# Kernel tuning notes

Hardware: AMD Instinct MI355X
Metric: run time of the kernel (lower is better)

Reference implementation:

```python
import jax, jax.numpy as jnp
import numpy as np

TOKEN_DIM = 4
EPS = 1e-6


def setup_inputs() -> dict:
    key = jax.random.key(0)
    k_x, k_w = jax.random.split(key)
    B, S, E = 8, 8192, 512
    EMB = 512
    x = jax.random.normal(k_x, (B, S, E), dtype=jnp.float32)
    ln_gamma = jnp.ones((E,), dtype=jnp.float32)
    ln_beta = jnp.zeros((E,), dtype=jnp.float32)
    # glorot-ish scale for the compression kernel [token_dim*E, EMB]
    W = jax.random.normal(k_w, (TOKEN_DIM * E, EMB), dtype=jnp.float32) * 0.02
    b = jnp.zeros((EMB,), dtype=jnp.float32)
    return {"x": x, "ln_gamma": ln_gamma, "ln_beta": ln_beta, "W": W, "b": b}


def reference(x, ln_gamma, ln_beta, W, b):
    B, S, E = x.shape
    # LayerNormalization over the feature axis (center + scale)
    mean = jnp.mean(x, axis=-1, keepdims=True)
    var = jnp.mean(jnp.square(x - mean), axis=-1, keepdims=True)
    h = (x - mean) * jax.lax.rsqrt(var + EPS) * ln_gamma + ln_beta
    # Divide: split sequence axis by token_dim and merge factor into feature axis
    # [B, S, E] -> [B, S//T, T*E]
    h = h.reshape(B, S // TOKEN_DIM, TOKEN_DIM * E)
    # Dense compression + exact gelu (keras 'gelu' uses erf form)
    out = jnp.einsum('bsf,fd->bsd', h, W) + b
    return jax.nn.gelu(out, approximate=False)
```

## Files before the change

kernel.cpp:

```cpp
#include <hip/hip_runtime.h>
#include <hip/hip_bf16.h>
#include <cstdint>

#define XROWS   65536
#define E       512
#define MROWS   16384
#define KDIM    2048
#define NDIM    512

typedef __attribute__((ext_vector_type(4))) float f32x4;
typedef __attribute__((ext_vector_type(8))) unsigned short u16x8;
typedef __attribute__((ext_vector_type(8))) __bf16 bf16x8;

__device__ __forceinline__ unsigned short f2bf(float f) {
  unsigned u = __builtin_bit_cast(unsigned, f);
  u += 0x7FFFu + ((u >> 16) & 1u);
  return (unsigned short)(u >> 16);
}

typedef const __attribute__((address_space(1))) unsigned char ga_u8;
typedef __attribute__((address_space(3))) unsigned char ls_u8;
__device__ __forceinline__ void gload16(const void* g, void* l) {
  __builtin_amdgcn_global_load_lds((ga_u8*)g, (ls_u8*)l, 16, 0, 0);
}

__global__ __launch_bounds__(256) void wt_kernel(const float* __restrict__ W,
                                                 unsigned short* __restrict__ WT) {
  __shared__ float tile[64][68];
  const int t  = threadIdx.x;
  const int bk = blockIdx.x >> 3;
  const int bn = blockIdx.x & 7;
  const int c4 = (t & 15) * 4;
#pragma unroll
  for (int i = 0; i < 4; ++i) {
    const int r = (t >> 4) + i * 16;
    const f32x4 v = *(const f32x4*)&W[(size_t)(bk * 64 + r) * NDIM + bn * 64 + c4];
    tile[r][c4 + 0] = v.x; tile[r][c4 + 1] = v.y;
    tile[r][c4 + 2] = v.z; tile[r][c4 + 3] = v.w;
  }
  __syncthreads();
#pragma unroll
  for (int j = 0; j < 2; ++j) {
    const int n  = j * 32 + (t >> 3);
    const int kb = (t & 7) * 8;
    u16x8 o;
#pragma unroll
    for (int q = 0; q < 8; ++q) o[q] = f2bf(tile[kb + q][n]);
    *(u16x8*)&WT[(size_t)(bn * 64 + n) * KDIM + bk * 64 + kb] = o;
  }
}

__global__ __launch_bounds__(256, 4) void ln_kernel(const float* __restrict__ x,
                                                    const float* __restrict__ gamma,
                                                    const float* __restrict__ beta,
                                                    unsigned short* __restrict__ h) {
  const int w = threadIdx.x >> 6, l = threadIdx.x & 63;
  const size_t row = (size_t)blockIdx.x * 4 + w;
  const float* xr = x + row * E + l * 8;
  const f32x4 v0 = *(const f32x4*)xr;
  const f32x4 v1 = *(const f32x4*)(xr + 4);
  float xv[8] = {v0.x, v0.y, v0.z, v0.w, v1.x, v1.y, v1.z, v1.w};
  float s = 0.f, q = 0.f;
#pragma unroll
  for (int j = 0; j < 8; ++j) { s += xv[j]; q += xv[j] * xv[j]; }
#pragma unroll
  for (int off = 32; off > 0; off >>= 1) {
    s += __shfl_xor(s, off);
    q += __shfl_xor(q, off);
  }
  const float mean = s * (1.0f / E);
  const float var  = q * (1.0f / E) - mean * mean;
  const float rstd = rsqrtf(var + 1e-6f);
  const f32x4 g0 = *(const f32x4*)(gamma + l * 8);
  const f32x4 g1 = *(const f32x4*)(gamma + l * 8 + 4);
  const f32x4 b0 = *(const f32x4*)(beta + l * 8);
  const f32x4 b1 = *(const f32x4*)(beta + l * 8 + 4);
  const float gv[8] = {g0.x, g0.y, g0.z, g0.w, g1.x, g1.y, g1.z, g1.w};
  const float bv[8] = {b0.x, b0.y, b0.z, b0.w, b1.x, b1.y, b1.z, b1.w};
  u16x8 o;
#pragma unroll
  for (int j = 0; j < 8; ++j) o[j] = f2bf((xv[j] - mean) * rstd * gv[j] + bv[j]);
  *(u16x8*)(h + row * E + l * 8) = o;
}

#define NT (KDIM / 64)

__global__ __launch_bounds__(256, 2) void gemm_kernel(const unsigned short* __restrict__ A,
                                                      const unsigned short* __restrict__ Bt,
                                                      const float* __restrict__ bias,
                                                      float* __restrict__ out) {
  __shared__ char smem[2 * 32768];
  const int tid = threadIdx.x;
  const int l = tid & 63, w = tid >> 6;
  const int l7 = l & 7, l15 = l & 15, lhi = l >> 4;
  const int wr = w >> 1, wc = w & 1;

  const int bn = blockIdx.x & 3;
  const int bm = blockIdx.x >> 2;
  const size_t arow0 = (size_t)bm * 128;
  const int    brow0 = bn * 128;

  const int srow = w * 8 + (l >> 3);
  const int swz  = (l7 * 16) ^ ((l >> 3) << 4);
  const char* gAb = (const char*)A  + ((size_t)(arow0 + srow) * KDIM) * 2 + swz;
  const char* gBb = (const char*)Bt + ((size_t)(brow0 + srow) * KDIM) * 2 + swz;

  auto stage = [&](int buf, int t) {
    char* base = smem + buf * 32768;
    const char* pa = gAb + (size_t)t * 128;
    const char* pb = gBb + (size_t)t * 128;
#pragma unroll
    for (int i = 0; i < 4; ++i) {
      gload16(pa + (size_t)i * 32 * KDIM * 2, base + (i * 32 + w * 8) * 128);
      gload16(pb + (size_t)i * 32 * KDIM * 2, base + 16384 + (i * 32 + w * 8) * 128);
    }
  };

  f32x4 acc[4][4];
#pragma unroll
  for (int m = 0; m < 4; ++m)
#pragma unroll
    for (int n = 0; n < 4; ++n) acc[m][n] = (f32x4){0.f, 0.f, 0.f, 0.f};

  const int cs0 = (lhi * 16) ^ (l7 * 16);

  stage(0, 0);
  __syncthreads();

  for (int t = 0; t < NT; ++t) {
    if (t + 1 < NT) stage((t + 1) & 1, t + 1);
    const char* Ab = smem + (t & 1) * 32768;
    const char* Bb = Ab + 16384;
#pragma unroll
    for (int kk = 0; kk < 2; ++kk) {
      const int co = cs0 ^ (kk * 64);
      bf16x8 av[4], bv[4];
#pragma unroll
      for (int m = 0; m < 4; ++m)
        av[m] = *(const bf16x8*)(Ab + (wr * 64 + m * 16 + l15) * 128 + co);
#pragma unroll
      for (int n = 0; n < 4; ++n)
        bv[n] = *(const bf16x8*)(Bb + (wc * 64 + n * 16 + l15) * 128 + co);
#pragma unroll
      for (int m = 0; m < 4; ++m)
#pragma unroll
        for (int n = 0; n < 4; ++n)
          acc[m][n] = __builtin_amdgcn_mfma_f32_16x16x32_bf16(av[m], bv[n], acc[m][n], 0, 0, 0);
    }
    __syncthreads();
  }

#pragma unroll
  for (int n = 0; n < 4; ++n) {
    const int col = brow0 + wc * 64 + n * 16 + l15;
    const float bb = bias[col];
#pragma unroll
    for (int m = 0; m < 4; ++m) {
      const size_t rbase = arow0 + wr * 64 + m * 16 + lhi * 4;
#pragma unroll
      for (int r = 0; r < 4; ++r) {
        const float v = acc[m][n][r] + bb;
        const float ge = 0.5f * v * (1.0f + erff(v * 0.70710678118654752f));
        out[(rbase + r) * NDIM + col] = ge;
      }
    }
  }
}

extern "C" void kernel_launch(void* const* d_in, const int* in_sizes, int n_in,
                              void* d_out, int out_size, void* d_ws, size_t ws_size,
                              hipStream_t stream) {
  const float* x     = (const float*)d_in[0];
  const float* gamma = (const float*)d_in[1];
  const float* beta  = (const float*)d_in[2];
  const float* W     = (const float*)d_in[3];
  const float* bias  = (const float*)d_in[4];
  float* out = (float*)d_out;

  unsigned short* WT = (unsigned short*)d_ws;
  const size_t wtBytes = (size_t)NDIM * KDIM * 2;
  unsigned short* h = (unsigned short*)((char*)d_ws + wtBytes);

  int NC = 1;
  while (NC < 64 && wtBytes + ((size_t)MROWS / NC) * KDIM * 2 > ws_size) NC <<= 1;
  const int Mc = MROWS / NC;

  wt_kernel<<<256, 256, 0, stream>>>(W, WT);
  for (int c = 0; c < NC; ++c) {
    const float* xc = x + (size_t)c * Mc * KDIM;
    ln_kernel<<<Mc, 256, 0, stream>>>(xc, gamma, beta, h);
    gemm_kernel<<<(Mc / 128) * 4, 256, 0, stream>>>(h, WT, bias,
                                                    out + (size_t)c * Mc * NDIM);
  }
}
```

Measured before the change: 87.92 us.

## Fuse LayerNorm apply into GEMM A-load, fold gamma/beta into weights and bias

The LayerNorm is split: a stats kernel writes only per-row scale and shift, and the GEMM loads fp32 x directly, normalizes and converts to bf16 into LDS while B streams in asynchronously. Gamma is folded into the transposed bf16 weights and beta@W plus b into a precomputed bias, so the bf16 h intermediate no longer has to be written and re-read. The GEMM tile changes to 64x256 with a register double-buffered A prefetch. The exact erf GELU is replaced by a sigmoid-style exp2 approximation, which is cheaper but may lose accuracy.

Measured after the change: 115.8 us. 31.7% more time.

```diff
diff --git a/kernel.cpp b/kernel.cpp
--- a/kernel.cpp
+++ b/kernel.cpp
@@ -7,8 +7,10 @@
 #define MROWS   16384
 #define KDIM    2048
 #define NDIM    512
+#define NT      32
 
 typedef __attribute__((ext_vector_type(4))) float f32x4;
+typedef __attribute__((ext_vector_type(2))) float f32x2;
 typedef __attribute__((ext_vector_type(8))) unsigned short u16x8;
 typedef __attribute__((ext_vector_type(8))) __bf16 bf16x8;
 
@@ -24,7 +26,15 @@
   __builtin_amdgcn_global_load_lds((ga_u8*)g, (ls_u8*)l, 16, 0, 0);
 }
 
+__device__ __forceinline__ float gelu_f(float v) {
+  float p = v * (2.3022083f + 0.1029432f * (v * v));
+  p = fminf(p, 80.0f);
+  const float Ee = exp2f(p);
+  return v * Ee * __builtin_amdgcn_rcpf(Ee + 1.0f);
+}
+
 __global__ __launch_bounds__(256) void wt_kernel(const float* __restrict__ W,
+                                                 const float* __restrict__ gamma,
                                                  unsigned short* __restrict__ WT) {
   __shared__ float tile[64][68];
   const int t  = threadIdx.x;
@@ -43,78 +53,89 @@
   for (int j = 0; j < 2; ++j) {
     const int n  = j * 32 + (t >> 3);
     const int kb = (t & 7) * 8;
+    const int kg0 = (bk & 7) * 64 + kb;
+    const f32x4 g0 = *(const f32x4*)(gamma + kg0);
+    const f32x4 g1 = *(const f32x4*)(gamma + kg0 + 4);
+    const float gg[8] = {g0.x, g0.y, g0.z, g0.w, g1.x, g1.y, g1.z, g1.w};
     u16x8 o;
 #pragma unroll
-    for (int q = 0; q < 8; ++q) o[q] = f2bf(tile[kb + q][n]);
+    for (int q = 0; q < 8; ++q) o[q] = f2bf(gg[q] * tile[kb + q][n]);
     *(u16x8*)&WT[(size_t)(bn * 64 + n) * KDIM + bk * 64 + kb] = o;
   }
 }
 
-__global__ __launch_bounds__(256, 4) void ln_kernel(const float* __restrict__ x,
-                                                    const float* __restrict__ gamma,
-                                                    const float* __restrict__ beta,
-                                                    unsigned short* __restrict__ h) {
+__global__ __launch_bounds__(256) void kbias1(const float* __restrict__ W,
+                                              const float* __restrict__ beta,
+                                              float* __restrict__ partial) {
+  const int bk = blockIdx.x, tid = threadIdx.x;
+  float a0 = 0.f, a1 = 0.f;
+  for (int k = 0; k < 64; ++k) {
+    const int kg = bk * 64 + k;
+    const float be = beta[kg & (E - 1)];
+    a0 += be * W[(size_t)kg * NDIM + tid];
+    a1 += be * W[(size_t)kg * NDIM + 256 + tid];
+  }
+  partial[bk * NDIM + tid] = a0;
+  partial[bk * NDIM + 256 + tid] = a1;
+}
+
+__global__ __launch_bounds__(256) void kbias2(const float* __restrict__ b,
+                                              const float* __restrict__ partial,
+                                              float* __restrict__ biasf) {
+  const int c = blockIdx.x * 256 + threadIdx.x;
+  float s = b[c];
+  for (int j = 0; j < 32; ++j) s += partial[j * NDIM + c];
+  biasf[c] = s;
+}
+
+__global__ __launch_bounds__(256, 4) void stats_kernel(const float* __restrict__ x,
+                                                       f32x2* __restrict__ stats) {
   const int w = threadIdx.x >> 6, l = threadIdx.x & 63;
   const size_t row = (size_t)blockIdx.x * 4 + w;
   const float* xr = x + row * E + l * 8;
   const f32x4 v0 = *(const f32x4*)xr;
   const f32x4 v1 = *(const f32x4*)(xr + 4);
-  float xv[8] = {v0.x, v0.y, v0.z, v0.w, v1.x, v1.y, v1.z, v1.w};
-  float s = 0.f, q = 0.f;
-#pragma unroll
-  for (int j = 0; j < 8; ++j) { s += xv[j]; q += xv[j] * xv[j]; }
+  float s = v0.x + v0.y + v0.z + v0.w + v1.x + v1.y + v1.z + v1.w;
+  float q = v0.x * v0.x + v0.y * v0.y + v0.z * v0.z + v0.w * v0.w
+          + v1.x * v1.x + v1.y * v1.y + v1.z * v1.z + v1.w * v1.w;
 #pragma unroll
   for (int off = 32; off > 0; off >>= 1) {
     s += __shfl_xor(s, off);
     q += __shfl_xor(q, off);
   }
-  const float mean = s * (1.0f / E);
-  const float var  = q * (1.0f / E) - mean * mean;
-  const float rstd = rsqrtf(var + 1e-6f);
-  const f32x4 g0 = *(const f32x4*)(gamma + l * 8);
-  const f32x4 g1 = *(const f32x4*)(gamma + l * 8 + 4);
-  const f32x4 b0 = *(const f32x4*)(beta + l * 8);
-  const f32x4 b1 = *(const f32x4*)(beta + l * 8 + 4);
-  const float gv[8] = {g0.x, g0.y, g0.z, g0.w, g1.x, g1.y, g1.z, g1.w};
-  const float bv[8] = {b0.x, b0.y, b0.z, b0.w, b1.x, b1.y, b1.z, b1.w};
-  u16x8 o;
-#pragma unroll
-  for (int j = 0; j < 8; ++j) o[j] = f2bf((xv[j] - mean) * rstd * gv[j] + bv[j]);
-  *(u16x8*)(h + row * E + l * 8) = o;
-}
-
-#define NT (KDIM / 64)
-
-__global__ __launch_bounds__(256, 2) void gemm_kernel(const unsigned short* __restrict__ A,
+  if (l == 0) {
+    const float mean = s * (1.0f / E);
+    const float var  = q * (1.0f / E) - mean * mean;
+    const float rs   = rsqrtf(var + 1e-6f);
+    f32x2 o; o.x = rs; o.y = -mean * rs;
+    stats[row] = o;
+  }
+}
+
+__global__ __launch_bounds__(256, 2) void gemm_kernel(const float* __restrict__ x,
+                                                      const f32x2* __restrict__ stats,
                                                       const unsigned short* __restrict__ Bt,
-                                                      const float* __restrict__ bias,
+                                                      const float* __restrict__ biasf,
                                                       float* __restrict__ out) {
-  __shared__ char smem[2 * 32768];
+  __shared__ char smem[2 * 40960];
   const int tid = threadIdx.x;
   const int l = tid & 63, w = tid >> 6;
   const int l7 = l & 7, l15 = l & 15, lhi = l >> 4;
-  const int wr = w >> 1, wc = w & 1;
-
-  const int bn = blockIdx.x & 3;
-  const int bm = blockIdx.x >> 2;
-  const size_t arow0 = (size_t)bm * 128;
-  const int    brow0 = bn * 128;
-
-  const int srow = w * 8 + (l >> 3);
-  const int swz  = (l7 * 16) ^ ((l >> 3) << 4);
-  const char* gAb = (const char*)A  + ((size_t)(arow0 + srow) * KDIM) * 2 + swz;
-  const char* gBb = (const char*)Bt + ((size_t)(brow0 + srow) * KDIM) * 2 + swz;
-
-  auto stage = [&](int buf, int t) {
-    char* base = smem + buf * 32768;
-    const char* pa = gAb + (size_t)t * 128;
-    const char* pb = gBb + (size_t)t * 128;
-#pragma unroll
-    for (int i = 0; i < 4; ++i) {
-      gload16(pa + (size_t)i * 32 * KDIM * 2, base + (i * 32 + w * 8) * 128);
-      gload16(pb + (size_t)i * 32 * KDIM * 2, base + 16384 + (i * 32 + w * 8) * 128);
-    }
-  };
+
+  const int bn = blockIdx.x & 1;
+  const int bm = blockIdx.x >> 1;
+  const size_t mrow0 = (size_t)bm * 64;
+  const int    ncol0 = bn * 256;
+
+  const int amrow = tid >> 3;
+  const int acol  = (tid & 7) * 8;
+  const float* gx = x + (mrow0 + amrow) * KDIM + acol;
+  const int sbase = (int)(mrow0 + amrow) * 4;
+  const int awz   = ((tid & 7) * 16) ^ ((amrow & 7) << 4);
+
+  const int bsrow = w * 8 + (l >> 3);
+  const int bswz  = (l7 * 16) ^ ((l >> 3) << 4);
+  const char* gB = (const char*)Bt + ((size_t)(ncol0 + bsrow) * KDIM) * 2 + bswz;
 
   f32x4 acc[4][4];
 #pragma unroll
@@ -124,44 +145,90 @@
 
   const int cs0 = (lhi * 16) ^ (l7 * 16);
 
-  stage(0, 0);
-  __syncthreads();
-
-  for (int t = 0; t < NT; ++t) {
-    if (t + 1 < NT) stage((t + 1) & 1, t + 1);
-    const char* Ab = smem + (t & 1) * 32768;
-    const char* Bb = Ab + 16384;
+  f32x4 xa0[4], xa1[4];
+  f32x2 st0[2], st1[2];
+
+  auto loadx = [&](f32x4* XA, f32x2* ST, int t) {
+    const float* p = gx + (size_t)t * 64;
+    XA[0] = *(const f32x4*)(p);
+    XA[1] = *(const f32x4*)(p + 4);
+    XA[2] = *(const f32x4*)(p + (size_t)32 * KDIM);
+    XA[3] = *(const f32x4*)(p + (size_t)32 * KDIM + 4);
+    ST[0] = stats[sbase + (t >> 3)];
+    ST[1] = stats[sbase + 128 + (t >> 3)];
+  };
+  auto writeA = [&](const f32x4* XA, const f32x2* ST, int t) {
+    char* ab = smem + (t & 1) * 40960;
+    u16x8 o;
+    float rs = ST[0].x, nm = ST[0].y;
+    o[0] = f2bf(XA[0].x * rs + nm); o[1] = f2bf(XA[0].y * rs + nm);
+    o[2] = f2bf(XA[0].z * rs + nm); o[3] = f2bf(XA[0].w * rs + nm);
+    o[4] = f2bf(XA[1].x * rs + nm); o[5] = f2bf(XA[1].y * rs + nm);
+    o[6] = f2bf(XA[1].z * rs + nm); o[7] = f2bf(XA[1].w * rs + nm);
+    *(u16x8*)(ab + amrow * 128 + awz) = o;
+    rs = ST[1].x; nm = ST[1].y;
+    o[0] = f2bf(XA[2].x * rs + nm); o[1] = f2bf(XA[2].y * rs + nm);
+    o[2] = f2bf(XA[2].z * rs + nm); o[3] = f2bf(XA[2].w * rs + nm);
+    o[4] = f2bf(XA[3].x * rs + nm); o[5] = f2bf(XA[3].y * rs + nm);
+    o[6] = f2bf(XA[3].z * rs + nm); o[7] = f2bf(XA[3].w * rs + nm);
+    *(u16x8*)(ab + (amrow + 32) * 128 + awz) = o;
+  };
+  auto stageB = [&](int t) {
+    char* bb = smem + (t & 1) * 40960 + 8192;
+    const char* pb = gB + (size_t)t * 128;
+#pragma unroll
+    for (int i = 0; i < 8; ++i)
+      gload16(pb + (size_t)i * 32 * KDIM * 2, bb + (i * 32 + w * 8) * 128);
+  };
+  auto mm = [&](int t) {
+    const char* Ab = smem + (t & 1) * 40960;
+    const char* Bb = Ab + 8192;
 #pragma unroll
     for (int kk = 0; kk < 2; ++kk) {
       const int co = cs0 ^ (kk * 64);
       bf16x8 av[4], bv[4];
 #pragma unroll
       for (int m = 0; m < 4; ++m)
-        av[m] = *(const bf16x8*)(Ab + (wr * 64 + m * 16 + l15) * 128 + co);
+        av[m] = *(const bf16x8*)(Ab + (m * 16 + l15) * 128 + co);
 #pragma unroll
       for (int n = 0; n < 4; ++n)
-        bv[n] = *(const bf16x8*)(Bb + (wc * 64 + n * 16 + l15) * 128 + co);
+        bv[n] = *(const bf16x8*)(Bb + (w * 64 + n * 16 + l15) * 128 + co);
 #pragma unroll
       for (int m = 0; m < 4; ++m)
 #pragma unroll
         for (int n = 0; n < 4; ++n)
           acc[m][n] = __builtin_amdgcn_mfma_f32_16x16x32_bf16(av[m], bv[n], acc[m][n], 0, 0, 0);
     }
+  };
+
+  loadx(xa0, st0, 0);
+  writeA(xa0, st0, 0);
+  stageB(0);
+  loadx(xa1, st1, 1);
+  __syncthreads();
+
+  for (int t = 0; t < NT; t += 2) {
+    if (t + 1 < NT) { stageB(t + 1); writeA(xa1, st1, t + 1); }
+    if (t + 2 < NT) loadx(xa0, st0, t + 2);
+    mm(t);
     __syncthreads();
+    if (t + 2 < NT) { stageB(t + 2); writeA(xa0, st0, t + 2); }
+    if (t + 3 < NT) loadx(xa1, st1, t + 3);
+    mm(t + 1);
+    __syncthreads();
   }
 
 #pragma unroll
   for (int n = 0; n < 4; ++n) {
-    const int col = brow0 + wc * 64 + n * 16 + l15;
-    const float bb = bias[col];
+    const int col = ncol0 + w * 64 + n * 16 + l15;
+    const float bb = biasf[col];
 #pragma unroll
     for (int m = 0; m < 4; ++m) {
-      const size_t rbase = arow0 + wr * 64 + m * 16 + lhi * 4;
+      const size_t rbase = mrow0 + m * 16 + lhi * 4;
 #pragma unroll
       for (int r = 0; r < 4; ++r) {
         const float v = acc[m][n][r] + bb;
-        const float ge = 0.5f * v * (1.0f + erff(v * 0.70710678118654752f));
-        out[(rbase + r) * NDIM + col] = ge;
+        out[(rbase + r) * NDIM + col] = gelu_f(v);
       }
     }
   }
@@ -174,22 +241,18 @@
   const float* gamma = (const float*)d_in[1];
   const float* beta  = (const float*)d_in[2];
   const float* W     = (const float*)d_in[3];
-  const float* bias  = (const float*)d_in[4];
+  const float* b     = (const float*)d_in[4];
   float* out = (float*)d_out;
 
-  unsigned short* WT = (unsigned short*)d_ws;
-  const size_t wtBytes = (size_t)NDIM * KDIM * 2;
-  unsigned short* h = (unsigned short*)((char*)d_ws + wtBytes);
-
-  int NC = 1;
-  while (NC < 64 && wtBytes + ((size_t)MROWS / NC) * KDIM * 2 > ws_size) NC <<= 1;
-  const int Mc = MROWS / NC;
-
-  wt_kernel<<<256, 256, 0, stream>>>(W, WT);
-  for (int c = 0; c < NC; ++c) {
-    const float* xc = x + (size_t)c * Mc * KDIM;
-    ln_kernel<<<Mc, 256, 0, stream>>>(xc, gamma, beta, h);
-    gemm_kernel<<<(Mc / 128) * 4, 256, 0, stream>>>(h, WT, bias,
-                                                    out + (size_t)c * Mc * NDIM);
-  }
-}
+  char* p = (char*)d_ws;
+  unsigned short* WT = (unsigned short*)p;            p += (size_t)NDIM * KDIM * 2;
+  f32x2* stats       = (f32x2*)p;                     p += (size_t)XROWS * 8;
+  float* partial     = (float*)p;                     p += (size_t)32 * NDIM * 4;
+  float* biasf       = (float*)p;
+
+  wt_kernel<<<256, 256, 0, stream>>>(W, gamma, WT);
+  kbias1<<<32, 256, 0, stream>>>(W, beta, partial);
+  kbias2<<<2, 256, 0, stream>>>(b, partial, biasf);
+  stats_kernel<<<XROWS / 4, 256, 0, stream>>>(x, stats);
+  gemm_kernel<<<(MROWS / 64) * 2, 256, 0, stream>>>(x, stats, WT, biasf, out);
+}
```
